# Kernel tuning notes

Measured on AMD Instinct MI355X. Metric: run time of the kernel, lower is better.

## Reference

```python
import jax, jax.numpy as jnp
import numpy as np

NGRAMS = 5


def _pair_idx():
    pairs = [(i, j) for i in range(NGRAMS) for j in range(i + 1, NGRAMS)]
    return (np.array([p[0] for p in pairs]), np.array([p[1] for p in pairs]))


def setup_inputs() -> dict:
    key = jax.random.key(0)
    ks = jax.random.split(key, 12)
    B, S, U = 8, 500, 128
    n = NGRAMS
    C = S // n          # 100 chunks
    F = n * (n - 1)     # 2 * C(n,2) = 20 edge-concat feature width
    H, DK = n, 2        # per-chunk MHA: 5 heads, key_dim=value_dim=2
    GH, GD = 4, U // 4  # graph MHA: 4 heads, key_dim=32
    s = 0.05
    inp = {
        'x': jax.random.normal(ks[0], (B, S, U), jnp.float32),
        'wq': s * jax.random.normal(ks[1], (C, F, H, DK), jnp.float32),
        'bq': jnp.zeros((C, H, DK), jnp.float32),
        'wk': s * jax.random.normal(ks[2], (C, F, H, DK), jnp.float32),
        'bk': jnp.zeros((C, H, DK), jnp.float32),
        'wv': s * jax.random.normal(ks[3], (C, F, H, DK), jnp.float32),
        'bv': jnp.zeros((C, H, DK), jnp.float32),
        'wo': s * jax.random.normal(ks[4], (C, H, DK, F), jnp.float32),
        'bo': jnp.zeros((C, F), jnp.float32),
        'pos': 0.02 * jax.random.normal(ks[5], (C, U), jnp.float32),
        'gwq': s * jax.random.normal(ks[6], (U, GH, GD), jnp.float32),
        'gbq': jnp.zeros((GH, GD), jnp.float32),
        'gwk': s * jax.random.normal(ks[7], (U, GH, GD), jnp.float32),
        'gbk': jnp.zeros((GH, GD), jnp.float32),
        'gwv': s * jax.random.normal(ks[8], (U, GH, GD), jnp.float32),
        'gbv': jnp.zeros((GH, GD), jnp.float32),
        'gwo': s * jax.random.normal(ks[9], (GH, GD, U), jnp.float32),
        'gbo': jnp.zeros((U,), jnp.float32),
    }
    return inp


def reference(x, wq, bq, wk, bk, wv, bv, wo, bo, pos,
              gwq, gbq, gwk, gbk, gwv, gbv, gwo, gbo):
    B, S, U = x.shape
    n = NGRAMS
    C = S // n
    ii, jj = _pair_idx()
    P = ii.shape[0]
    # [B,S,U] -> [B,U,S] -> chunks [B,U,C,n]
    xt = jnp.transpose(x, (0, 2, 1)).reshape(B, U, C, n)
    # edge construction: concat of every node pair per chunk -> [B,U,C,2P]
    H_edges = jnp.stack([xt[..., ii], xt[..., jj]], axis=-1).reshape(B, U, C, 2 * P)
    Ht = jnp.transpose(H_edges, (0, 2, 1, 3))  # [B,C,U,F], attention seq axis = U
    dk = wq.shape[-1]
    scale = 1.0 / jnp.sqrt(jnp.asarray(dk, x.dtype))
    q = (jnp.einsum('bcuf,cfhd->bcuhd', Ht, wq) + bq[None, :, None]) * scale
    k = jnp.einsum('bcuf,cfhd->bcuhd', Ht, wk) + bk[None, :, None]
    v = jnp.einsum('bcuf,cfhd->bcuhd', Ht, wv) + bv[None, :, None]
    scores = jnp.einsum('bcuhd,bcvhd->bchuv', q, k)
    attn = jax.nn.softmax(scores, axis=-1)
    o = jnp.einsum('bchuv,bcvhd->bcuhd', attn, v)
    mha_out = jnp.einsum('bcuhd,chdf->bcuf', o, wo) + bo[None, :, None]
    alpha = jax.nn.leaky_relu(Ht + mha_out, negative_slope=0.3)  # [B,C,U,F]
    # stack + reduce_mean over edge-feature axis, transpose -> [B,C,U]
    g = jnp.mean(alpha, axis=-1)
    g = g + pos[None]  # learned position embedding over C
    # graph-level self-attention over the C axis
    gdk = gwq.shape[-1]
    gscale = 1.0 / jnp.sqrt(jnp.asarray(gdk, x.dtype))
    gq = (jnp.einsum('bcu,uhd->bchd', g, gwq) + gbq) * gscale
    gk = jnp.einsum('bcu,uhd->bchd', g, gwk) + gbk
    gv = jnp.einsum('bcu,uhd->bchd', g, gwv) + gbv
    gs = jnp.einsum('bqhd,bkhd->bhqk', gq, gk)
    ga = jax.nn.softmax(gs, axis=-1)
    go = jnp.einsum('bhqk,bkhd->bqhd', ga, gv)
    g_attn = jnp.einsum('bqhd,hdu->bqu', go, gwo) + gbo
    return g + g_attn  # [B, C, U]
```

## Files before the change

kernel.cpp:

```cpp
#include <hip/hip_runtime.h>

#define NB  8
#define SS  500
#define UU  128
#define NG  5
#define CC  100
#define PP  10
#define FF  20
#define HH  5
#define HD  10
#define GHH 4
#define GDD 32

__global__ __launch_bounds__(640) void k1_chunk_mha(
    const float* __restrict__ x,   const float* __restrict__ wq,
    const float* __restrict__ bq,  const float* __restrict__ wk,
    const float* __restrict__ bk,  const float* __restrict__ wv,
    const float* __restrict__ bv,  const float* __restrict__ wo,
    const float* __restrict__ bo,  const float* __restrict__ pos,
    const float* __restrict__ gwq, const float* __restrict__ gbq,
    const float* __restrict__ gwk, const float* __restrict__ gbk,
    const float* __restrict__ gwv, const float* __restrict__ gbv,
    float* __restrict__ g_out, float* __restrict__ gq_out,
    float* __restrict__ gk_out, float* __restrict__ gv_out)
{
    const int bc = blockIdx.x;
    const int b  = bc / CC, c = bc % CC;
    const int u  = threadIdx.x & 127;
    const int h  = threadIdx.x >> 7;

    __shared__ float4 s_kv[UU][HH];
    __shared__ float2 s_o[UU][HH];
    __shared__ float  s_part[HH][UU];
    __shared__ float  s_g[UU];
    __shared__ float  s_red[3][HH][UU];

    float xv[NG];
    const float* xb = x + (size_t)b * SS * UU + (size_t)c * NG * UU + u;
#pragma unroll
    for (int t = 0; t < NG; ++t) xv[t] = xb[t * UU];

    const int II[PP] = {0,0,0,0,1,1,1,2,2,3};
    const int JJ[PP] = {1,2,3,4,2,3,4,3,4,4};
    float ht[FF];
#pragma unroll
    for (int p = 0; p < PP; ++p) { ht[2*p] = xv[II[p]]; ht[2*p+1] = xv[JJ[p]]; }

    const int cb = c * (FF * HD) + 2 * h;
    float q0 = bq[c*HD + 2*h], q1 = bq[c*HD + 2*h + 1];
    float k0 = bk[c*HD + 2*h], k1 = bk[c*HD + 2*h + 1];
    float v0 = bv[c*HD + 2*h], v1 = bv[c*HD + 2*h + 1];
#pragma unroll
    for (int f = 0; f < FF; ++f) {
        const float hf = ht[f];
        q0 = fmaf(hf, wq[cb + f*HD],     q0);
        q1 = fmaf(hf, wq[cb + f*HD + 1], q1);
        k0 = fmaf(hf, wk[cb + f*HD],     k0);
        k1 = fmaf(hf, wk[cb + f*HD + 1], k1);
        v0 = fmaf(hf, wv[cb + f*HD],     v0);
        v1 = fmaf(hf, wv[cb + f*HD + 1], v1);
    }
    s_kv[u][h] = make_float4(k0, k1, v0, v1);
    __syncthreads();

    const float scale = 0.7071067811865476f;
    q0 *= scale; q1 *= scale;
    float l = 0.f, o0 = 0.f, o1 = 0.f;
#pragma unroll 4
    for (int vi = 0; vi < UU; ++vi) {
        const float4 kvv = s_kv[vi][h];
        const float s = fmaf(q0, kvv.x, q1 * kvv.y);
        const float e = __expf(s);
        l += e;
        o0 = fmaf(e, kvv.z, o0);
        o1 = fmaf(e, kvv.w, o1);
    }
    const float inv = 1.f / l;
    s_o[u][h] = make_float2(o0 * inv, o1 * inv);
    __syncthreads();

    float ov[HD];
#pragma unroll
    for (int h2 = 0; h2 < HH; ++h2) {
        const float2 t2 = s_o[u][h2];
        ov[2*h2] = t2.x; ov[2*h2+1] = t2.y;
    }
    const float* woc = wo + c * (HD * FF);
    float part = 0.f;
#pragma unroll
    for (int j = 0; j < 4; ++j) {
        const int f = h * 4 + j;
        float acc = bo[c*FF + f];
#pragma unroll
        for (int hd = 0; hd < HD; ++hd) acc = fmaf(ov[hd], woc[hd*FF + f], acc);
        const float a = ht[f] + acc;
        part += (a > 0.f) ? a : 0.3f * a;
    }
    s_part[h][u] = part;
    __syncthreads();

    if (h == 0) {
        const float gsum = s_part[0][u] + s_part[1][u] + s_part[2][u]
                         + s_part[3][u] + s_part[4][u];
        const float g = gsum * (1.f / FF) + pos[c*UU + u];
        s_g[u] = g;
        g_out[(size_t)bc*UU + u] = g;
    }
    __syncthreads();

    const int st = h * 26, en = (h == 4) ? UU : st + 26;
    float aq = (h == 0) ? gbq[u] : 0.f;
    float ak = (h == 0) ? gbk[u] : 0.f;
    float av = (h == 0) ? gbv[u] : 0.f;
    for (int u2 = st; u2 < en; ++u2) {
        const float gu = s_g[u2];
        aq = fmaf(gu, gwq[u2*UU + u], aq);
        ak = fmaf(gu, gwk[u2*UU + u], ak);
        av = fmaf(gu, gwv[u2*UU + u], av);
    }
    s_red[0][h][u] = aq; s_red[1][h][u] = ak; s_red[2][h][u] = av;
    __syncthreads();

    if (h < 3) {
        const float sum = s_red[h][0][u] + s_red[h][1][u] + s_red[h][2][u]
                        + s_red[h][3][u] + s_red[h][4][u];
        if (h == 0)      gq_out[(size_t)bc*UU + u] = sum * 0.17677669529663687f;
        else if (h == 1) gk_out[(size_t)bc*UU + u] = sum;
        else             gv_out[(size_t)bc*UU + u] = sum;
    }
}

__global__ __launch_bounds__(128) void k2_graph(
    const float* __restrict__ gq, const float* __restrict__ gk,
    const float* __restrict__ gv, const float* __restrict__ gwo,
    const float* __restrict__ gbo, float* __restrict__ out)
{
    const int bq = blockIdx.x;
    const int b  = bq / CC;
    const int t  = threadIdx.x;

    __shared__ float s_q[UU];
    __shared__ float s_e[GHH][CC];
    __shared__ float s_o[UU];

    const float gval = out[(size_t)bq*UU + t];
    s_q[t] = gq[(size_t)bq*UU + t];
    __syncthreads();

    if (t < CC) {
        const float4* krow = (const float4*)(gk + ((size_t)b*CC + t)*UU);
        const float4* q4   = (const float4*)s_q;
#pragma unroll
        for (int hh = 0; hh < GHH; ++hh) {
            float s = 0.f;
#pragma unroll
            for (int i = 0; i < 8; ++i) {
                const float4 kf = krow[hh*8 + i];
                const float4 qf = q4[hh*8 + i];
                s = fmaf(qf.x, kf.x, s); s = fmaf(qf.y, kf.y, s);
                s = fmaf(qf.z, kf.z, s); s = fmaf(qf.w, kf.w, s);
            }
            s_e[hh][t] = __expf(s);
        }
    }
    __syncthreads();

    {
        const int h = t >> 5;
        const float* vcol = gv + (size_t)b*CC*UU + t;
        float l = 0.f, o = 0.f;
#pragma unroll 4
        for (int k = 0; k < CC; ++k) {
            const float e = s_e[h][k];
            l += e;
            o = fmaf(e, vcol[(size_t)k*UU], o);
        }
        s_o[t] = o / l;
    }
    __syncthreads();

    float acc = gbo[t];
#pragma unroll 4
    for (int hd = 0; hd < UU; ++hd)
        acc = fmaf(s_o[hd], gwo[hd*UU + t], acc);
    out[(size_t)bq*UU + t] = gval + acc;
}

extern "C" void kernel_launch(void* const* d_in, const int* in_sizes, int n_in,
                              void* d_out, int out_size, void* d_ws, size_t ws_size,
                              hipStream_t stream)
{
    (void)in_sizes; (void)n_in; (void)out_size; (void)ws_size;
    const float* x   = (const float*)d_in[0];
    const float* wq  = (const float*)d_in[1];
    const float* bq  = (const float*)d_in[2];
    const float* wk  = (const float*)d_in[3];
    const float* bk  = (const float*)d_in[4];
    const float* wv  = (const float*)d_in[5];
    const float* bv  = (const float*)d_in[6];
    const float* wo  = (const float*)d_in[7];
    const float* bo  = (const float*)d_in[8];
    const float* pos = (const float*)d_in[9];
    const float* gwq = (const float*)d_in[10];
    const float* gbq = (const float*)d_in[11];
    const float* gwk = (const float*)d_in[12];
    const float* gbk = (const float*)d_in[13];
    const float* gwv = (const float*)d_in[14];
    const float* gbv = (const float*)d_in[15];
    const float* gwo = (const float*)d_in[16];
    const float* gbo = (const float*)d_in[17];
    float* out = (float*)d_out;
    float* ws  = (float*)d_ws;

    float* gq_ws = ws;
    float* gk_ws = ws + 102400;
    float* gv_ws = ws + 204800;

    k1_chunk_mha<<<NB*CC, 640, 0, stream>>>(x, wq, bq, wk, bk, wv, bv, wo, bo,
        pos, gwq, gbq, gwk, gbk, gwv, gbv, out, gq_ws, gk_ws, gv_ws);
    k2_graph<<<NB*CC, 128, 0, stream>>>(gq_ws, gk_ws, gv_ws, gwo, gbo, out);
}
```

Baseline: 156.3 us.

## Remap chunk MHA to quad-per-token with bf16 K/V and split graph kernel work

The chunk attention kernel is reorganised: each token gets four lanes, and each lane computes one of Q, K or V for all heads. K and V are stored in shared memory as packed bf16, each lane sweeps a quarter of the keys, and the partial softmax sums are combined with DPP quad reductions. This drops the shared-memory round trips for the output projection. The graph kernel now uses 256 threads and splits the score, value and output projection loops in half with shared-memory reductions. The changes aim for more parallelism and less shared traffic, but the bf16 rounding of K and V adds precision loss.

```diff
diff --git a/kernel.cpp b/kernel.cpp
--- a/kernel.cpp
+++ b/kernel.cpp
@@ -5,14 +5,31 @@
 #define UU  128
 #define NG  5
 #define CC  100
-#define PP  10
 #define FF  20
 #define HH  5
 #define HD  10
-#define GHH 4
-#define GDD 32
-
-__global__ __launch_bounds__(640) void k1_chunk_mha(
+
+__device__ __constant__ const int EI[FF] =
+    {0,1, 0,2, 0,3, 0,4, 1,2, 1,3, 1,4, 2,3, 2,4, 3,4};
+
+template <int CTRL>
+__device__ __forceinline__ float qperm(float x) {
+    return __int_as_float(__builtin_amdgcn_update_dpp(
+        0, __float_as_int(x), CTRL, 0xF, 0xF, true));
+}
+__device__ __forceinline__ float quad_sum(float x) {
+    x += qperm<0xB1>(x);
+    x += qperm<0x4E>(x);
+    return x;
+}
+__device__ __forceinline__ unsigned bf16pk(float a, float b) {
+    unsigned ua = __float_as_uint(a), ub = __float_as_uint(b);
+    ua = (ua + 0x7FFFu + ((ua >> 16) & 1u)) >> 16;
+    ub = (ub + 0x7FFFu + ((ub >> 16) & 1u)) & 0xFFFF0000u;
+    return ua | ub;
+}
+
+__global__ __launch_bounds__(512, 6) void k1_chunk_mha(
     const float* __restrict__ x,   const float* __restrict__ wq,
     const float* __restrict__ bq,  const float* __restrict__ wk,
     const float* __restrict__ bk,  const float* __restrict__ wv,
@@ -24,113 +41,141 @@
     float* __restrict__ g_out, float* __restrict__ gq_out,
     float* __restrict__ gk_out, float* __restrict__ gv_out)
 {
-    const int bc = blockIdx.x;
-    const int b  = bc / CC, c = bc % CC;
-    const int u  = threadIdx.x & 127;
-    const int h  = threadIdx.x >> 7;
-
-    __shared__ float4 s_kv[UU][HH];
-    __shared__ float2 s_o[UU][HH];
-    __shared__ float  s_part[HH][UU];
-    __shared__ float  s_g[UU];
-    __shared__ float  s_red[3][HH][UU];
+    const int bc  = blockIdx.x;
+    const int b   = bc / CC, c = bc % CC;
+    const int tid = threadIdx.x;
+    const int u   = tid >> 2;
+    const int vq  = tid & 3;
+
+    __shared__ uint4 s_k4[HH * 32];
+    __shared__ uint4 s_v4[HH * 32];
+    __shared__ float s_g[UU];
+    __shared__ float s_gr[4][3][UU];
+    unsigned* s_k = (unsigned*)s_k4;
+    unsigned* s_v = (unsigned*)s_v4;
 
     float xv[NG];
     const float* xb = x + (size_t)b * SS * UU + (size_t)c * NG * UU + u;
 #pragma unroll
     for (int t = 0; t < NG; ++t) xv[t] = xb[t * UU];
 
-    const int II[PP] = {0,0,0,0,1,1,1,2,2,3};
-    const int JJ[PP] = {1,2,3,4,2,3,4,3,4,4};
-    float ht[FF];
-#pragma unroll
-    for (int p = 0; p < PP; ++p) { ht[2*p] = xv[II[p]]; ht[2*p+1] = xv[JJ[p]]; }
-
-    const int cb = c * (FF * HD) + 2 * h;
-    float q0 = bq[c*HD + 2*h], q1 = bq[c*HD + 2*h + 1];
-    float k0 = bk[c*HD + 2*h], k1 = bk[c*HD + 2*h + 1];
-    float v0 = bv[c*HD + 2*h], v1 = bv[c*HD + 2*h + 1];
+    const float* wsel = (vq == 1) ? wk : (vq == 2) ? wv : wq;
+    const float* bsel = (vq == 1) ? bk : (vq == 2) ? bv : bq;
+    float p[HD];
+    {
+        const float2* bs2 = (const float2*)(bsel + c * HD);
+#pragma unroll
+        for (int d2 = 0; d2 < 5; ++d2) {
+            const float2 t2 = bs2[d2];
+            p[2*d2] = t2.x; p[2*d2+1] = t2.y;
+        }
+        const float2* w2 = (const float2*)(wsel + c * (FF * HD));
+#pragma unroll
+        for (int f = 0; f < FF; ++f) {
+            const float hf = xv[EI[f]];
+#pragma unroll
+            for (int d2 = 0; d2 < 5; ++d2) {
+                const float2 t2 = w2[f*5 + d2];
+                p[2*d2]   = fmaf(hf, t2.x, p[2*d2]);
+                p[2*d2+1] = fmaf(hf, t2.y, p[2*d2+1]);
+            }
+        }
+    }
+    if (vq == 1) {
+#pragma unroll
+        for (int h = 0; h < HH; ++h) s_k[h*UU + u] = bf16pk(p[2*h], p[2*h+1]);
+    } else if (vq == 2) {
+#pragma unroll
+        for (int h = 0; h < HH; ++h) s_v[h*UU + u] = bf16pk(p[2*h], p[2*h+1]);
+    }
+    const float scale = 0.7071067811865476f;
+    float q0[HH], q1[HH];
+#pragma unroll
+    for (int h = 0; h < HH; ++h) {
+        q0[h] = qperm<0x00>(p[2*h])   * scale;
+        q1[h] = qperm<0x00>(p[2*h+1]) * scale;
+    }
+    __syncthreads();
+
+    float l[HH], o0[HH], o1[HH];
+#pragma unroll
+    for (int h = 0; h < HH; ++h) { l[h] = 0.f; o0[h] = 0.f; o1[h] = 0.f; }
+#pragma unroll
+    for (int h = 0; h < HH; ++h) {
+#pragma unroll
+        for (int j = 0; j < 8; ++j) {
+            const int i4 = h*32 + vq*8 + ((j + 2*vq) & 7);
+            const uint4 kk = s_k4[i4];
+            const uint4 vv = s_v4[i4];
+            const unsigned kw[4] = {kk.x, kk.y, kk.z, kk.w};
+            const unsigned vw[4] = {vv.x, vv.y, vv.z, vv.w};
+#pragma unroll
+            for (int m = 0; m < 4; ++m) {
+                const float k0 = __uint_as_float(kw[m] << 16);
+                const float k1 = __uint_as_float(kw[m] & 0xFFFF0000u);
+                const float s  = fmaf(q0[h], k0, q1[h] * k1);
+                const float e  = __expf(s);
+                l[h] += e;
+                o0[h] = fmaf(e, __uint_as_float(vw[m] << 16),         o0[h]);
+                o1[h] = fmaf(e, __uint_as_float(vw[m] & 0xFFFF0000u), o1[h]);
+            }
+        }
+    }
+    float o[HD];
+#pragma unroll
+    for (int h = 0; h < HH; ++h) {
+        const float L  = quad_sum(l[h]);
+        const float O0 = quad_sum(o0[h]);
+        const float O1 = quad_sum(o1[h]);
+        const float inv = 1.f / L;
+        o[2*h] = O0 * inv; o[2*h+1] = O1 * inv;
+    }
+
+    const float* woc = wo + c * (HD * FF);
+    const float* boc = bo + c * FF;
+    float gsum = 0.f;
 #pragma unroll
     for (int f = 0; f < FF; ++f) {
-        const float hf = ht[f];
-        q0 = fmaf(hf, wq[cb + f*HD],     q0);
-        q1 = fmaf(hf, wq[cb + f*HD + 1], q1);
-        k0 = fmaf(hf, wk[cb + f*HD],     k0);
-        k1 = fmaf(hf, wk[cb + f*HD + 1], k1);
-        v0 = fmaf(hf, wv[cb + f*HD],     v0);
-        v1 = fmaf(hf, wv[cb + f*HD + 1], v1);
-    }
-    s_kv[u][h] = make_float4(k0, k1, v0, v1);
-    __syncthreads();
-
-    const float scale = 0.7071067811865476f;
-    q0 *= scale; q1 *= scale;
-    float l = 0.f, o0 = 0.f, o1 = 0.f;
+        float acc = boc[f];
+#pragma unroll
+        for (int hd = 0; hd < HD; ++hd) acc = fmaf(o[hd], woc[hd*FF + f], acc);
+        const float a = xv[EI[f]] + acc;
+        gsum += (a > 0.f) ? a : 0.3f * a;
+    }
+    const float g = gsum * (1.f / FF) + pos[c*UU + u];
+    if (vq == 0) {
+        g_out[(size_t)bc*UU + u] = g;
+        s_g[u] = g;
+    }
+    __syncthreads();
+
+    const int ug = tid & 127, pp = tid >> 7;
+    float aq = 0.f, ak = 0.f, av = 0.f;
 #pragma unroll 4
-    for (int vi = 0; vi < UU; ++vi) {
-        const float4 kvv = s_kv[vi][h];
-        const float s = fmaf(q0, kvv.x, q1 * kvv.y);
-        const float e = __expf(s);
-        l += e;
-        o0 = fmaf(e, kvv.z, o0);
-        o1 = fmaf(e, kvv.w, o1);
-    }
-    const float inv = 1.f / l;
-    s_o[u][h] = make_float2(o0 * inv, o1 * inv);
-    __syncthreads();
-
-    float ov[HD];
-#pragma unroll
-    for (int h2 = 0; h2 < HH; ++h2) {
-        const float2 t2 = s_o[u][h2];
-        ov[2*h2] = t2.x; ov[2*h2+1] = t2.y;
-    }
-    const float* woc = wo + c * (HD * FF);
-    float part = 0.f;
-#pragma unroll
-    for (int j = 0; j < 4; ++j) {
-        const int f = h * 4 + j;
-        float acc = bo[c*FF + f];
-#pragma unroll
-        for (int hd = 0; hd < HD; ++hd) acc = fmaf(ov[hd], woc[hd*FF + f], acc);
-        const float a = ht[f] + acc;
-        part += (a > 0.f) ? a : 0.3f * a;
-    }
-    s_part[h][u] = part;
-    __syncthreads();
-
-    if (h == 0) {
-        const float gsum = s_part[0][u] + s_part[1][u] + s_part[2][u]
-                         + s_part[3][u] + s_part[4][u];
-        const float g = gsum * (1.f / FF) + pos[c*UU + u];
-        s_g[u] = g;
-        g_out[(size_t)bc*UU + u] = g;
-    }
-    __syncthreads();
-
-    const int st = h * 26, en = (h == 4) ? UU : st + 26;
-    float aq = (h == 0) ? gbq[u] : 0.f;
-    float ak = (h == 0) ? gbk[u] : 0.f;
-    float av = (h == 0) ? gbv[u] : 0.f;
-    for (int u2 = st; u2 < en; ++u2) {
+    for (int i = 0; i < 32; ++i) {
+        const int u2 = pp*32 + i;
         const float gu = s_g[u2];
-        aq = fmaf(gu, gwq[u2*UU + u], aq);
-        ak = fmaf(gu, gwk[u2*UU + u], ak);
-        av = fmaf(gu, gwv[u2*UU + u], av);
-    }
-    s_red[0][h][u] = aq; s_red[1][h][u] = ak; s_red[2][h][u] = av;
-    __syncthreads();
-
-    if (h < 3) {
-        const float sum = s_red[h][0][u] + s_red[h][1][u] + s_red[h][2][u]
-                        + s_red[h][3][u] + s_red[h][4][u];
-        if (h == 0)      gq_out[(size_t)bc*UU + u] = sum * 0.17677669529663687f;
-        else if (h == 1) gk_out[(size_t)bc*UU + u] = sum;
-        else             gv_out[(size_t)bc*UU + u] = sum;
-    }
-}
-
-__global__ __launch_bounds__(128) void k2_graph(
+        aq = fmaf(gu, gwq[u2*UU + ug], aq);
+        ak = fmaf(gu, gwk[u2*UU + ug], ak);
+        av = fmaf(gu, gwv[u2*UU + ug], av);
+    }
+    s_gr[pp][0][ug] = aq; s_gr[pp][1][ug] = ak; s_gr[pp][2][ug] = av;
+    __syncthreads();
+
+    if (pp < 3) {
+        const float s = s_gr[0][pp][ug] + s_gr[1][pp][ug]
+                      + s_gr[2][pp][ug] + s_gr[3][pp][ug];
+        if (pp == 0)
+            gq_out[(size_t)bc*UU + ug] = (s + gbq[ug]) * 0.17677669529663687f;
+        else if (pp == 1)
+            gk_out[(size_t)bc*UU + ug] = s + gbk[ug];
+        else
+            gv_out[(size_t)bc*UU + ug] = s + gbv[ug];
+    }
+}
+
+#define GHH 4
+__global__ __launch_bounds__(256) void k2_graph(
     const float* __restrict__ gq, const float* __restrict__ gk,
     const float* __restrict__ gv, const float* __restrict__ gwo,
     const float* __restrict__ gbo, float* __restrict__ out)
@@ -141,49 +186,69 @@
 
     __shared__ float s_q[UU];
     __shared__ float s_e[GHH][CC];
+    __shared__ float s_pa[2][UU];
+    __shared__ float s_pl[2][UU];
     __shared__ float s_o[UU];
-
-    const float gval = out[(size_t)bq*UU + t];
-    s_q[t] = gq[(size_t)bq*UU + t];
-    __syncthreads();
-
-    if (t < CC) {
-        const float4* krow = (const float4*)(gk + ((size_t)b*CC + t)*UU);
+    __shared__ float s_p3[2][UU];
+
+    float gval = 0.f;
+    if (t < UU) {
+        gval  = out[(size_t)bq*UU + t];
+        s_q[t] = gq[(size_t)bq*UU + t];
+    }
+    __syncthreads();
+
+    if (t < 200) {
+        const int k  = (t < 100) ? t : t - 100;
+        const int h0 = (t < 100) ? 0 : 2;
+        const float4* krow = (const float4*)(gk + ((size_t)b*CC + k)*UU);
         const float4* q4   = (const float4*)s_q;
 #pragma unroll
-        for (int hh = 0; hh < GHH; ++hh) {
+        for (int hh = 0; hh < 2; ++hh) {
+            const int h = h0 + hh;
             float s = 0.f;
 #pragma unroll
             for (int i = 0; i < 8; ++i) {
-                const float4 kf = krow[hh*8 + i];
-                const float4 qf = q4[hh*8 + i];
+                const float4 kf = krow[h*8 + i];
+                const float4 qf = q4[h*8 + i];
                 s = fmaf(qf.x, kf.x, s); s = fmaf(qf.y, kf.y, s);
                 s = fmaf(qf.z, kf.z, s); s = fmaf(qf.w, kf.w, s);
             }
-            s_e[hh][t] = __expf(s);
+            s_e[h][k] = __expf(s);
         }
     }
     __syncthreads();
 
     {
-        const int h = t >> 5;
-        const float* vcol = gv + (size_t)b*CC*UU + t;
+        const int d = t & 127, kh = t >> 7, h = d >> 5;
+        const float* vcol = gv + (size_t)b*CC*UU + d;
         float l = 0.f, o = 0.f;
-#pragma unroll 4
-        for (int k = 0; k < CC; ++k) {
+#pragma unroll 5
+        for (int i = 0; i < 50; ++i) {
+            const int k = kh*50 + i;
             const float e = s_e[h][k];
             l += e;
             o = fmaf(e, vcol[(size_t)k*UU], o);
         }
-        s_o[t] = o / l;
-    }
-    __syncthreads();
-
-    float acc = gbo[t];
+        s_pa[kh][d] = o; s_pl[kh][d] = l;
+    }
+    __syncthreads();
+    if (t < UU) s_o[t] = (s_pa[0][t] + s_pa[1][t]) / (s_pl[0][t] + s_pl[1][t]);
+    __syncthreads();
+
+    {
+        const int u = t & 127, half = t >> 7;
+        float acc = 0.f;
 #pragma unroll 4
-    for (int hd = 0; hd < UU; ++hd)
-        acc = fmaf(s_o[hd], gwo[hd*UU + t], acc);
-    out[(size_t)bq*UU + t] = gval + acc;
+        for (int i = 0; i < 64; ++i) {
+            const int hd = half*64 + i;
+            acc = fmaf(s_o[hd], gwo[hd*UU + u], acc);
+        }
+        s_p3[half][u] = acc;
+    }
+    __syncthreads();
+    if (t < UU)
+        out[(size_t)bq*UU + t] = gval + s_p3[0][t] + s_p3[1][t] + gbo[t];
 }
 
 extern "C" void kernel_launch(void* const* d_in, const int* in_sizes, int n_in,
@@ -216,7 +281,7 @@
     float* gk_ws = ws + 102400;
     float* gv_ws = ws + 204800;
 
-    k1_chunk_mha<<<NB*CC, 640, 0, stream>>>(x, wq, bq, wk, bk, wv, bv, wo, bo,
+    k1_chunk_mha<<<NB*CC, 512, 0, stream>>>(x, wq, bq, wk, bk, wv, bv, wo, bo,
         pos, gwq, gbq, gwk, gbk, gwv, gbv, out, gq_ws, gk_ws, gv_ws);
-    k2_graph<<<NB*CC, 128, 0, stream>>>(gq_ws, gk_ws, gv_ws, gwo, gbo, out);
-}
+    k2_graph<<<NB*CC, 256, 0, stream>>>(gq_ws, gk_ws, gv_ws, gwo, gbo, out);
+}
```

Result: slower. 164.7 us (+5.4%).
